# Kernel tuning notes

Measured on AMD Instinct MI355X. Metric: run time of the kernel, lower is better.

## Reference

```python
import math
import jax, jax.numpy as jnp
import numpy as np

BS, H, S, DK = 16, 8, 1024, 128
NEG = -1e32

def setup_inputs() -> dict:
    key = jax.random.key(0)
    kq, kk, kv = jax.random.split(key, 3)
    q = jax.random.normal(kq, (BS, H, S, DK), dtype=jnp.float32)
    k = jax.random.normal(kk, (BS, H, S, DK), dtype=jnp.float32)
    v = jax.random.normal(kv, (BS, H, S, DK), dtype=jnp.float32)
    # causal mask: 1 where attending allowed (lower-triangular incl. diagonal)
    mask = jnp.tril(jnp.ones((S, S), dtype=jnp.int32))[None, None, :, :]
    return {"q": q, "k": k, "v": v, "mask": mask, "k_index": 5}


def reference(q, k, v, mask, k_index):
    d_k = q.shape[-1]
    bs, h, S, _ = q.shape
    # raw scaled scores [bs, h, S, S]
    scores = jnp.einsum("bhqd,bhkd->bhqk", q, k) / math.sqrt(d_k)
    scores = jnp.where(mask == 0, NEG, scores)
    scores = jax.nn.softmax(scores, axis=-1)
    # 'sparseattn' branch: keep rows < k_index intact; for later rows keep only
    # entries >= the k_index-th largest value, then re-softmax everything.
    scores_a = scores[:, :, :k_index, :]
    scores_b = scores[:, :, k_index:, :]
    kth = jax.lax.top_k(scores_b, k_index)[0][..., -1:]  # k-th largest per row
    scores_b = jnp.where(scores_b - kth >= 0, scores_b, NEG)
    scores = jnp.concatenate([scores_a, scores_b], axis=2)
    scores = jax.nn.softmax(scores, axis=-1)
    # zero_pad: zero out attention of the first position
    pad_zero = jnp.zeros((bs, h, 1, S), dtype=scores.dtype)
    scores = jnp.concatenate([pad_zero, scores[:, :, 1:, :]], axis=2)
    # dropout prob is 0.0 -> identity
    out = jnp.einsum("bhqk,bhkd->bhqd", scores, v)
    return out
```

## Files before the change

### kernel.cpp

```cpp
#include <hip/hip_runtime.h>
#include <math.h>

#define BSZ 16
#define NH  8
#define SEQ 1024
#define DK  128
#define QB  64
#define KB  64
#define NT  256
#define TOPK 5
#define NC   8
#define EPS_REF 4e-3f

typedef _Float16 half8 __attribute__((ext_vector_type(8)));
typedef float f32x4 __attribute__((ext_vector_type(4)));

#define INV2P11 4.8828125e-4f

__device__ __forceinline__ void ins8p(float (&t)[NC], int (&ti)[NC], float x, int xi) {
    #pragma unroll
    for (int i = 0; i < NC; ++i) {
        bool gt = x > t[i];
        float tv = t[i]; int tiv = ti[i];
        t[i]  = gt ? x  : tv;
        ti[i] = gt ? xi : tiv;
        x  = gt ? tv  : x;
        xi = gt ? tiv : xi;
    }
}

__device__ __forceinline__ float ref_score(const float* __restrict__ qp,
                                           const float* __restrict__ kp,
                                           float scale) {
    const float4* q4 = (const float4*)qp;
    const float4* k4 = (const float4*)kp;
    float a0 = 0.f;
    #pragma unroll 8
    for (int c = 0; c < DK / 4; ++c) {
        float4 kx = k4[c];
        float4 t0 = q4[c];
        a0 = fmaf(kx.x, t0.x, a0);
        a0 = fmaf(kx.y, t0.y, a0);
        a0 = fmaf(kx.z, t0.z, a0);
        a0 = fmaf(kx.w, t0.w, a0);
    }
    return a0 * scale;
}

__launch_bounds__(NT, 4)
__global__ void attn_topk_mfma(const float* __restrict__ Q,
                               const float* __restrict__ Km,
                               const float* __restrict__ V,
                               const int* __restrict__ kidx_ptr,
                               float* __restrict__ out)
{
    const int bh   = blockIdx.y;
    const int qb   = ((int)gridDim.x - 1 - (int)blockIdx.x) * QB;
    const int tid  = threadIdx.x;
    const int lane = tid & 63;
    const int w    = tid >> 6;
    const int c    = lane & 15;
    const int grp  = lane >> 4;
    const int Kv   = *kidx_ptr;

    __shared__ __align__(16) _Float16 khi [KB * DK];
    __shared__ __align__(16) _Float16 kmid[KB * DK];
    __shared__ float s_coef[4][16][NC];
    __shared__ int   s_idx [4][16][NC];
    __shared__ float s_ext [4][16];
    __shared__ int   s_cnt [4][16];
    __shared__ float s_sv  [DK];
    __shared__ float s_svp [2][DK];

    if (qb == 0) {
        const float* vb = V + (size_t)bh * SEQ * DK;
        const int col = tid & 127, hf = tid >> 7;
        float a = 0.f;
        #pragma unroll 8
        for (int j = hf * 512; j < hf * 512 + 512; ++j)
            a += vb[(size_t)j * DK + col];
        s_svp[hf][col] = a;
        __syncthreads();
        if (tid < DK) s_sv[tid] = s_svp[0][tid] + s_svp[1][tid];
    }

    const int qrow = qb + w * 16 + c;
    const float scale = 0.08838834764831845f;
    half8 qhi[4], qmid[4];
    {
        const float* qp = Q + ((size_t)bh * SEQ + qrow) * DK;
        #pragma unroll
        for (int d = 0; d < 4; ++d) {
            const float4* p4 = (const float4*)(qp + d * 32 + grp * 8);
            float4 f0 = p4[0], f1 = p4[1];
            float v[8] = {f0.x, f0.y, f0.z, f0.w, f1.x, f1.y, f1.z, f1.w};
            #pragma unroll
            for (int j = 0; j < 8; ++j) {
                _Float16 h = (_Float16)v[j];
                float r = v[j] - (float)h;
                qhi[d][j]  = h;
                qmid[d][j] = (_Float16)(r * 2048.0f);
            }
        }
    }

    float t[NC]; int ti[NC];
    #pragma unroll
    for (int i = 0; i < NC; ++i) { t[i] = -INFINITY; ti[i] = 0; }
    float Zr = 0.f;

    const int qmax_w = qb + w * 16 + 15;
    const int ntile  = qb / KB + 1;
    const float* kb_g = Km + (size_t)bh * SEQ * DK;

    for (int kt = 0; kt < ntile; ++kt) {
        __syncthreads();
        {
            const float* src = kb_g + (size_t)kt * KB * DK;
            #pragma unroll
            for (int it = 0; it < 4; ++it) {
                int e   = it * 2048 + tid * 8;
                int row = e >> 7;
                int d0  = e & 127;
                const float4* g4 = (const float4*)(src + (size_t)row * DK + d0);
                float4 f0 = g4[0], f1 = g4[1];
                float v[8] = {f0.x, f0.y, f0.z, f0.w, f1.x, f1.y, f1.z, f1.w};
                half8 hv, mv;
                #pragma unroll
                for (int j = 0; j < 8; ++j) {
                    _Float16 h = (_Float16)v[j];
                    float r = v[j] - (float)h;
                    hv[j] = h;
                    mv[j] = (_Float16)(r * 2048.0f);
                }
                int off = row * 256 + ((d0 * 2) ^ ((row & 7) << 4));
                *(half8*)((char*)khi  + off) = hv;
                *(half8*)((char*)kmid + off) = mv;
            }
        }
        __syncthreads();

        const int kbase_t = kt * KB;
        #pragma unroll
        for (int fr = 0; fr < 4; ++fr) {
            if (kbase_t + fr * 16 <= qmax_w) {
                f32x4 a1 = {0.f, 0.f, 0.f, 0.f};
                f32x4 a2 = {0.f, 0.f, 0.f, 0.f};
                const int kr    = fr * 16 + c;
                const int rbase = kr * 256;
                const int sw    = (kr & 7) << 4;
                #pragma unroll
                for (int d = 0; d < 4; ++d) {
                    int off = rbase + (((d * 64) + grp * 16) ^ sw);
                    half8 ah = *(const half8*)((const char*)khi  + off);
                    half8 am = *(const half8*)((const char*)kmid + off);
                    a1 = __builtin_amdgcn_mfma_f32_16x16x32_f16(ah, qhi[d],  a1, 0, 0, 0);
                    a2 = __builtin_amdgcn_mfma_f32_16x16x32_f16(ah, qmid[d], a2, 0, 0, 0);
                    a2 = __builtin_amdgcn_mfma_f32_16x16x32_f16(am, qhi[d],  a2, 0, 0, 0);
                }
                #pragma unroll
                for (int r = 0; r < 4; ++r) {
                    float s = fmaf(a2[r], INV2P11, a1[r]) * scale;
                    int kg = kbase_t + fr * 16 + grp * 4 + r;
                    if (kg <= qrow) {
                        if (s > t[NC - 1]) {
                            float mo = t[0];
                            ins8p(t, ti, s, kg);
                            float mn = t[0];
                            if (mn != mo) Zr *= __expf(mo - mn);
                        }
                        Zr += __expf(s - t[0]);
                    }
                }
            }
        }
    }

    #pragma unroll
    for (int off = 16; off < 64; off <<= 1) {
        float zo = __shfl_xor(Zr, off, 64);
        float to[NC]; int io[NC];
        #pragma unroll
        for (int i = 0; i < NC; ++i) {
            to[i] = __shfl_xor(t[i], off, 64);
            io[i] = __shfl_xor(ti[i], off, 64);
        }
        float ms = t[0], mo = to[0];
        float mN = fmaxf(ms, mo);
        float fs = (ms == mN) ? 1.f : __expf(ms - mN);
        float fo = (mo == mN) ? 1.f : __expf(mo - mN);
        Zr = Zr * fs + zo * fo;
        #pragma unroll
        for (int i = 0; i < NC; ++i) ins8p(t, ti, to[i], io[i]);
    }

    if (qrow >= Kv && (t[TOPK - 1] - t[TOPK]) < EPS_REF) {
        const float* qrp = Q + ((size_t)bh * SEQ + qrow) * DK;
        float rv0 = -INFINITY, rv1 = -INFINITY;
        int   ri0 = ti[grp * 2], ri1 = ti[grp * 2 + 1];
        if (t[grp * 2] != -INFINITY)
            rv0 = ref_score(qrp, Km + ((size_t)bh * SEQ + ri0) * DK, scale);
        if (t[grp * 2 + 1] != -INFINITY)
            rv1 = ref_score(qrp, Km + ((size_t)bh * SEQ + ri1) * DK, scale);
        float av[NC]; int ai[NC];
        #pragma unroll
        for (int j = 0; j < NC; ++j) {
            int src = (lane & 15) | ((j >> 1) << 4);
            av[j] = __shfl((j & 1) ? rv1 : rv0, src, 64);
            ai[j] = __shfl((j & 1) ? ri1 : ri0, src, 64);
        }
        #pragma unroll
        for (int a = 1; a < NC; ++a) {
            #pragma unroll
            for (int b = NC - 1; b > 0; --b) {
                if (av[b] > av[b - 1]) {
                    float tv = av[b]; av[b] = av[b - 1]; av[b - 1] = tv;
                    int   tj = ai[b]; ai[b] = ai[b - 1]; ai[b - 1] = tj;
                }
            }
        }
        #pragma unroll
        for (int i = 0; i < NC; ++i) { t[i] = av[i]; ti[i] = ai[i]; }
    }

    if (grp == 0) {
        const float m1 = t[0];
        const float invZ = 1.f / Zr;
        if (qrow >= Kv) {
            float p[NC];
            #pragma unroll
            for (int i = 0; i < NC; ++i)
                p[i] = (t[i] == -INFINITY) ? -1.f : expf(t[i] - m1) * invZ;
            const float kth_p = p[TOPK - 1];
            int n = 0; float wsum = 0.f;
            #pragma unroll
            for (int i = 0; i < NC; ++i) {
                if (t[i] != -INFINITY && p[i] >= kth_p) {
                    float wv = expf(p[i]);
                    s_coef[w][c][n] = wv;
                    s_idx [w][c][n] = ti[i];
                    wsum += wv;
                    ++n;
                }
            }
            float iw = 1.f / wsum;
            for (int i = 0; i < n; ++i) s_coef[w][c][i] *= iw;
            s_cnt[w][c] = n;
            s_ext[w][c] = 0.f;
        } else if (qrow == 0) {
            s_cnt[w][c] = 0;
            s_ext[w][c] = 0.f;
        } else {
            float z2 = (float)(SEQ - 1 - qrow);
            float ex[TOPK];
            #pragma unroll
            for (int i = 0; i < TOPK; ++i) {
                if (i <= qrow) {
                    float p = expf(t[i] - m1) * invZ;
                    ex[i] = expf(p);
                    z2 += ex[i];
                } else ex[i] = 0.f;
            }
            float iz = 1.f / z2;
            #pragma unroll
            for (int i = 0; i < TOPK; ++i) {
                if (i <= qrow) {
                    s_coef[w][c][i] = (ex[i] - 1.f) * iz;
                    s_idx [w][c][i] = ti[i];
                }
            }
            s_cnt[w][c] = qrow + 1;
            s_ext[w][c] = iz;
        }
    }
    __syncthreads();

    const float* vb = V + (size_t)bh * SEQ * DK;
    #pragma unroll 2
    for (int r = 0; r < 16; ++r) {
        const int row = qb + w * 16 + r;
        const int n = s_cnt[w][r];
        const float e = s_ext[w][r];
        float a0, a1v;
        if (e != 0.f) { a0 = e * s_sv[2 * lane]; a1v = e * s_sv[2 * lane + 1]; }
        else          { a0 = 0.f; a1v = 0.f; }
        for (int i = 0; i < n; ++i) {
            float cf = s_coef[w][r][i];
            int   ji = s_idx [w][r][i];
            const float2 v2 = *(const float2*)(vb + (size_t)ji * DK + 2 * lane);
            a0  = fmaf(cf, v2.x, a0);
            a1v = fmaf(cf, v2.y, a1v);
        }
        float2 o; o.x = a0; o.y = a1v;
        *(float2*)(out + ((size_t)bh * SEQ + row) * DK + 2 * lane) = o;
    }
}

extern "C" void kernel_launch(void* const* d_in, const int* in_sizes, int n_in,
                              void* d_out, int out_size, void* d_ws, size_t ws_size,
                              hipStream_t stream) {
    const float* q    = (const float*)d_in[0];
    const float* k    = (const float*)d_in[1];
    const float* v    = (const float*)d_in[2];
    const int*   kidx = (const int*)d_in[4];
    float* out = (float*)d_out;

    dim3 grid(SEQ / QB, BSZ * NH);
    attn_topk_mfma<<<grid, NT, 0, stream>>>(q, k, v, kidx, out);
}
```

Before: 511.7 us.

## Prefetch next K tile into registers, specialize diagonal tile, use exp2 softmax

```diff
diff --git a/kernel.cpp b/kernel.cpp
--- a/kernel.cpp
+++ b/kernel.cpp
@@ -10,7 +10,8 @@
 #define NT  256
 #define TOPK 5
 #define NC   8
-#define EPS_REF 4e-3f
+#define EPS_REF 6e-3f
+#define LOG2E 1.4426950408889634f
 
 typedef _Float16 half8 __attribute__((ext_vector_type(8)));
 typedef float f32x4 __attribute__((ext_vector_type(4)));
@@ -60,7 +61,7 @@
     const int lane = tid & 63;
     const int w    = tid >> 6;
     const int c    = lane & 15;
-    const int grp  = lane >> 4;
+    const int g16  = lane >> 4;
     const int Kv   = *kidx_ptr;
 
     __shared__ __align__(16) _Float16 khi [KB * DK];
@@ -85,13 +86,14 @@
     }
 
     const int qrow = qb + w * 16 + c;
-    const float scale = 0.08838834764831845f;
+    const float scale  = 0.08838834764831845f;
+    const float scale2 = 0.08838834764831845f * LOG2E;
     half8 qhi[4], qmid[4];
     {
         const float* qp = Q + ((size_t)bh * SEQ + qrow) * DK;
         #pragma unroll
         for (int d = 0; d < 4; ++d) {
-            const float4* p4 = (const float4*)(qp + d * 32 + grp * 8);
+            const float4* p4 = (const float4*)(qp + d * 32 + g16 * 8);
             float4 f0 = p4[0], f1 = p4[1];
             float v[8] = {f0.x, f0.y, f0.z, f0.w, f1.x, f1.y, f1.z, f1.w};
             #pragma unroll
@@ -107,23 +109,28 @@
     float t[NC]; int ti[NC];
     #pragma unroll
     for (int i = 0; i < NC; ++i) { t[i] = -INFINITY; ti[i] = 0; }
-    float Zr = 0.f;
-
-    const int qmax_w = qb + w * 16 + 15;
+    float Zp0 = 0.f, Zp1 = 0.f, Zp2 = 0.f, Zp3 = 0.f;
+
     const int ntile  = qb / KB + 1;
     const float* kb_g = Km + (size_t)bh * SEQ * DK;
+
+    float4 pf[8];
+    {
+        const float* sp = kb_g + (size_t)(lane >> 2) * DK + w * 32 + (lane & 3) * 8;
+        #pragma unroll
+        for (int it = 0; it < 4; ++it) {
+            const float4* p4 = (const float4*)(sp + (size_t)it * 16 * DK);
+            pf[2 * it]     = p4[0];
+            pf[2 * it + 1] = p4[1];
+        }
+    }
 
     for (int kt = 0; kt < ntile; ++kt) {
         __syncthreads();
         {
-            const float* src = kb_g + (size_t)kt * KB * DK;
             #pragma unroll
             for (int it = 0; it < 4; ++it) {
-                int e   = it * 2048 + tid * 8;
-                int row = e >> 7;
-                int d0  = e & 127;
-                const float4* g4 = (const float4*)(src + (size_t)row * DK + d0);
-                float4 f0 = g4[0], f1 = g4[1];
+                float4 f0 = pf[2 * it], f1 = pf[2 * it + 1];
                 float v[8] = {f0.x, f0.y, f0.z, f0.w, f1.x, f1.y, f1.z, f1.w};
                 half8 hv, mv;
                 #pragma unroll
@@ -133,48 +140,87 @@
                     hv[j] = h;
                     mv[j] = (_Float16)(r * 2048.0f);
                 }
-                int off = row * 256 + ((d0 * 2) ^ ((row & 7) << 4));
+                const int off = it * 4096 + tid * 16;
                 *(half8*)((char*)khi  + off) = hv;
                 *(half8*)((char*)kmid + off) = mv;
             }
         }
+        if (kt + 1 < ntile) {
+            const float* sp = kb_g + (size_t)((kt + 1) * KB + (lane >> 2)) * DK
+                            + w * 32 + (lane & 3) * 8;
+            #pragma unroll
+            for (int it = 0; it < 4; ++it) {
+                const float4* p4 = (const float4*)(sp + (size_t)it * 16 * DK);
+                pf[2 * it]     = p4[0];
+                pf[2 * it + 1] = p4[1];
+            }
+        }
         __syncthreads();
 
         const int kbase_t = kt * KB;
+        const bool lastT = (kt == ntile - 1);
         #pragma unroll
         for (int fr = 0; fr < 4; ++fr) {
-            if (kbase_t + fr * 16 <= qmax_w) {
+            const bool doFull = !lastT || (fr < w);
+            const bool doDiag = lastT && (fr == w);
+            if (doFull | doDiag) {
                 f32x4 a1 = {0.f, 0.f, 0.f, 0.f};
                 f32x4 a2 = {0.f, 0.f, 0.f, 0.f};
-                const int kr    = fr * 16 + c;
-                const int rbase = kr * 256;
-                const int sw    = (kr & 7) << 4;
+                const int rbase = fr * 4096 + c * 64 + g16 * 16;
                 #pragma unroll
                 for (int d = 0; d < 4; ++d) {
-                    int off = rbase + (((d * 64) + grp * 16) ^ sw);
+                    const int off = rbase + d * 1024;
                     half8 ah = *(const half8*)((const char*)khi  + off);
                     half8 am = *(const half8*)((const char*)kmid + off);
                     a1 = __builtin_amdgcn_mfma_f32_16x16x32_f16(ah, qhi[d],  a1, 0, 0, 0);
                     a2 = __builtin_amdgcn_mfma_f32_16x16x32_f16(ah, qmid[d], a2, 0, 0, 0);
                     a2 = __builtin_amdgcn_mfma_f32_16x16x32_f16(am, qhi[d],  a2, 0, 0, 0);
                 }
-                #pragma unroll
-                for (int r = 0; r < 4; ++r) {
-                    float s = fmaf(a2[r], INV2P11, a1[r]) * scale;
-                    int kg = kbase_t + fr * 16 + grp * 4 + r;
-                    if (kg <= qrow) {
+                if (doFull) {
+                    #pragma unroll
+                    for (int r = 0; r < 4; ++r) {
+                        float s = fmaf(a2[r], INV2P11, a1[r]) * scale2;
+                        int kg = kbase_t + fr * 16 + g16 * 4 + r;
                         if (s > t[NC - 1]) {
                             float mo = t[0];
                             ins8p(t, ti, s, kg);
                             float mn = t[0];
-                            if (mn != mo) Zr *= __expf(mo - mn);
+                            if (mn != mo) {
+                                float f = exp2f(mo - mn);
+                                Zp0 *= f; Zp1 *= f; Zp2 *= f; Zp3 *= f;
+                            }
                         }
-                        Zr += __expf(s - t[0]);
+                        float e = exp2f(s - t[0]);
+                        if (r == 0) Zp0 += e; else if (r == 1) Zp1 += e;
+                        else if (r == 2) Zp2 += e; else Zp3 += e;
                     }
-                }
-            }
-        }
-    }
+                } else {
+                    #pragma unroll
+                    for (int r = 0; r < 4; ++r) {
+                        float s = fmaf(a2[r], INV2P11, a1[r]) * scale2;
+                        int kgl = g16 * 4 + r;
+                        if (kgl <= c) {
+                            int kg = kbase_t + fr * 16 + kgl;
+                            if (s > t[NC - 1]) {
+                                float mo = t[0];
+                                ins8p(t, ti, s, kg);
+                                float mn = t[0];
+                                if (mn != mo) {
+                                    float f = exp2f(mo - mn);
+                                    Zp0 *= f; Zp1 *= f; Zp2 *= f; Zp3 *= f;
+                                }
+                            }
+                            float e = exp2f(s - t[0]);
+                            if (r == 0) Zp0 += e; else if (r == 1) Zp1 += e;
+                            else if (r == 2) Zp2 += e; else Zp3 += e;
+                        }
+                    }
+                }
+            }
+        }
+    }
+
+    float Zr = (Zp0 + Zp1) + (Zp2 + Zp3);
 
     #pragma unroll
     for (int off = 16; off < 64; off <<= 1) {
@@ -187,8 +233,8 @@
         }
         float ms = t[0], mo = to[0];
         float mN = fmaxf(ms, mo);
-        float fs = (ms == mN) ? 1.f : __expf(ms - mN);
-        float fo = (mo == mN) ? 1.f : __expf(mo - mN);
+        float fs = (ms == mN) ? 1.f : exp2f(ms - mN);
+        float fo = (mo == mN) ? 1.f : exp2f(mo - mN);
         Zr = Zr * fs + zo * fo;
         #pragma unroll
         for (int i = 0; i < NC; ++i) ins8p(t, ti, to[i], io[i]);
@@ -197,10 +243,10 @@
     if (qrow >= Kv && (t[TOPK - 1] - t[TOPK]) < EPS_REF) {
         const float* qrp = Q + ((size_t)bh * SEQ + qrow) * DK;
         float rv0 = -INFINITY, rv1 = -INFINITY;
-        int   ri0 = ti[grp * 2], ri1 = ti[grp * 2 + 1];
-        if (t[grp * 2] != -INFINITY)
+        int   ri0 = ti[g16 * 2], ri1 = ti[g16 * 2 + 1];
+        if (t[g16 * 2] != -INFINITY)
             rv0 = ref_score(qrp, Km + ((size_t)bh * SEQ + ri0) * DK, scale);
-        if (t[grp * 2 + 1] != -INFINITY)
+        if (t[g16 * 2 + 1] != -INFINITY)
             rv1 = ref_score(qrp, Km + ((size_t)bh * SEQ + ri1) * DK, scale);
         float av[NC]; int ai[NC];
         #pragma unroll
@@ -220,17 +266,17 @@
             }
         }
         #pragma unroll
-        for (int i = 0; i < NC; ++i) { t[i] = av[i]; ti[i] = ai[i]; }
-    }
-
-    if (grp == 0) {
+        for (int i = 0; i < NC; ++i) { t[i] = av[i] * LOG2E; ti[i] = ai[i]; }
+    }
+
+    if (g16 == 0) {
         const float m1 = t[0];
         const float invZ = 1.f / Zr;
         if (qrow >= Kv) {
             float p[NC];
             #pragma unroll
             for (int i = 0; i < NC; ++i)
-                p[i] = (t[i] == -INFINITY) ? -1.f : expf(t[i] - m1) * invZ;
+                p[i] = (t[i] == -INFINITY) ? -1.f : exp2f(t[i] - m1) * invZ;
             const float kth_p = p[TOPK - 1];
             int n = 0; float wsum = 0.f;
             #pragma unroll
@@ -256,7 +302,7 @@
             #pragma unroll
             for (int i = 0; i < TOPK; ++i) {
                 if (i <= qrow) {
-                    float p = expf(t[i] - m1) * invZ;
+                    float p = exp2f(t[i] - m1) * invZ;
                     ex[i] = expf(p);
                     z2 += ex[i];
                 } else ex[i] = 0.f;
```

After: 540.2 us. 5.6% more time.

## Drop online max rescaling, fold scale and log2e into Q, shrink K tile to 32

Applied to the files above, without the earlier changes.

```diff
diff --git a/kernel.cpp b/kernel.cpp
--- a/kernel.cpp
+++ b/kernel.cpp
@@ -6,18 +6,19 @@
 #define SEQ 1024
 #define DK  128
 #define QB  64
-#define KB  64
+#define KB  32
 #define NT  256
 #define TOPK 5
-#define NC   8
-#define EPS_REF 4e-3f
+#define NC   6
+#define EPS_REF 6e-3f
+#define LOG2E 1.4426950408889634f
 
 typedef _Float16 half8 __attribute__((ext_vector_type(8)));
 typedef float f32x4 __attribute__((ext_vector_type(4)));
 
 #define INV2P11 4.8828125e-4f
 
-__device__ __forceinline__ void ins8p(float (&t)[NC], int (&ti)[NC], float x, int xi) {
+__device__ __forceinline__ void ins6p(float (&t)[NC], int (&ti)[NC], float x, int xi) {
     #pragma unroll
     for (int i = 0; i < NC; ++i) {
         bool gt = x > t[i];
@@ -47,7 +48,7 @@
     return a0 * scale;
 }
 
-__launch_bounds__(NT, 4)
+__launch_bounds__(NT, 6)
 __global__ void attn_topk_mfma(const float* __restrict__ Q,
                                const float* __restrict__ Km,
                                const float* __restrict__ V,
@@ -60,7 +61,7 @@
     const int lane = tid & 63;
     const int w    = tid >> 6;
     const int c    = lane & 15;
-    const int grp  = lane >> 4;
+    const int g16  = lane >> 4;
     const int Kv   = *kidx_ptr;
 
     __shared__ __align__(16) _Float16 khi [KB * DK];
@@ -85,19 +86,21 @@
     }
 
     const int qrow = qb + w * 16 + c;
-    const float scale = 0.08838834764831845f;
+    const float scale  = 0.08838834764831845f;
+    const float scale2 = 0.08838834764831845f * LOG2E;
     half8 qhi[4], qmid[4];
     {
         const float* qp = Q + ((size_t)bh * SEQ + qrow) * DK;
         #pragma unroll
         for (int d = 0; d < 4; ++d) {
-            const float4* p4 = (const float4*)(qp + d * 32 + grp * 8);
+            const float4* p4 = (const float4*)(qp + d * 32 + g16 * 8);
             float4 f0 = p4[0], f1 = p4[1];
             float v[8] = {f0.x, f0.y, f0.z, f0.w, f1.x, f1.y, f1.z, f1.w};
             #pragma unroll
             for (int j = 0; j < 8; ++j) {
-                _Float16 h = (_Float16)v[j];
-                float r = v[j] - (float)h;
+                float x = v[j] * scale2;
+                _Float16 h = (_Float16)x;
+                float r = x - (float)h;
                 qhi[d][j]  = h;
                 qmid[d][j] = (_Float16)(r * 2048.0f);
             }
@@ -107,10 +110,10 @@
     float t[NC]; int ti[NC];
     #pragma unroll
     for (int i = 0; i < NC; ++i) { t[i] = -INFINITY; ti[i] = 0; }
-    float Zr = 0.f;
-
-    const int qmax_w = qb + w * 16 + 15;
-    const int ntile  = qb / KB + 1;
+    float Zp0 = 0.f, Zp1 = 0.f, Zp2 = 0.f, Zp3 = 0.f;
+
+    const int R      = (qb >> 4) + w;
+    const int ntile  = qb / KB + 2;
     const float* kb_g = Km + (size_t)bh * SEQ * DK;
 
     for (int kt = 0; kt < ntile; ++kt) {
@@ -118,12 +121,10 @@
         {
             const float* src = kb_g + (size_t)kt * KB * DK;
             #pragma unroll
-            for (int it = 0; it < 4; ++it) {
-                int e   = it * 2048 + tid * 8;
-                int row = e >> 7;
-                int d0  = e & 127;
-                const float4* g4 = (const float4*)(src + (size_t)row * DK + d0);
-                float4 f0 = g4[0], f1 = g4[1];
+            for (int o = 0; o < 2; ++o) {
+                const float* sp = src + (size_t)(o * 16 + c) * DK + w * 32 + g16 * 8;
+                const float4* p4 = (const float4*)sp;
+                float4 f0 = p4[0], f1 = p4[1];
                 float v[8] = {f0.x, f0.y, f0.z, f0.w, f1.x, f1.y, f1.z, f1.w};
                 half8 hv, mv;
                 #pragma unroll
@@ -133,81 +134,75 @@
                     hv[j] = h;
                     mv[j] = (_Float16)(r * 2048.0f);
                 }
-                int off = row * 256 + ((d0 * 2) ^ ((row & 7) << 4));
+                const int off = o * 4096 + w * 1024 + lane * 16;
                 *(half8*)((char*)khi  + off) = hv;
                 *(half8*)((char*)kmid + off) = mv;
             }
         }
         __syncthreads();
 
-        const int kbase_t = kt * KB;
-        #pragma unroll
-        for (int fr = 0; fr < 4; ++fr) {
-            if (kbase_t + fr * 16 <= qmax_w) {
-                f32x4 a1 = {0.f, 0.f, 0.f, 0.f};
-                f32x4 a2 = {0.f, 0.f, 0.f, 0.f};
-                const int kr    = fr * 16 + c;
-                const int rbase = kr * 256;
-                const int sw    = (kr & 7) << 4;
-                #pragma unroll
-                for (int d = 0; d < 4; ++d) {
-                    int off = rbase + (((d * 64) + grp * 16) ^ sw);
-                    half8 ah = *(const half8*)((const char*)khi  + off);
-                    half8 am = *(const half8*)((const char*)kmid + off);
-                    a1 = __builtin_amdgcn_mfma_f32_16x16x32_f16(ah, qhi[d],  a1, 0, 0, 0);
-                    a2 = __builtin_amdgcn_mfma_f32_16x16x32_f16(ah, qmid[d], a2, 0, 0, 0);
-                    a2 = __builtin_amdgcn_mfma_f32_16x16x32_f16(am, qhi[d],  a2, 0, 0, 0);
-                }
-                #pragma unroll
-                for (int r = 0; r < 4; ++r) {
-                    float s = fmaf(a2[r], INV2P11, a1[r]) * scale;
-                    int kg = kbase_t + fr * 16 + grp * 4 + r;
-                    if (kg <= qrow) {
-                        if (s > t[NC - 1]) {
-                            float mo = t[0];
-                            ins8p(t, ti, s, kg);
-                            float mn = t[0];
-                            if (mn != mo) Zr *= __expf(mo - mn);
-                        }
-                        Zr += __expf(s - t[0]);
-                    }
-                }
-            }
-        }
-    }
+        #pragma unroll
+        for (int fr = 0; fr < 2; ++fr) {
+            const int F = kt * 2 + fr;
+            if (F > R) break;
+            const bool diag = (F == R);
+            f32x4 a1 = {0.f, 0.f, 0.f, 0.f};
+            f32x4 a2 = {0.f, 0.f, 0.f, 0.f};
+            const int rbase = fr * 4096 + lane * 16;
+            #pragma unroll
+            for (int d = 0; d < 4; ++d) {
+                const int off = rbase + d * 1024;
+                half8 ah = *(const half8*)((const char*)khi  + off);
+                half8 am = *(const half8*)((const char*)kmid + off);
+                a1 = __builtin_amdgcn_mfma_f32_16x16x32_f16(ah, qhi[d],  a1, 0, 0, 0);
+                a2 = __builtin_amdgcn_mfma_f32_16x16x32_f16(ah, qmid[d], a2, 0, 0, 0);
+                a2 = __builtin_amdgcn_mfma_f32_16x16x32_f16(am, qhi[d],  a2, 0, 0, 0);
+            }
+            #pragma unroll
+            for (int r = 0; r < 4; ++r) {
+                float s = fmaf(a2[r], INV2P11, a1[r]);
+                int kgl = g16 * 4 + r;
+                if (!diag || kgl <= c) {
+                    int kg = F * 16 + kgl;
+                    if (s > t[NC - 1]) ins6p(t, ti, s, kg);
+                    float e = exp2f(s);
+                    if (r == 0) Zp0 += e; else if (r == 1) Zp1 += e;
+                    else if (r == 2) Zp2 += e; else Zp3 += e;
+                }
+            }
+        }
+    }
+
+    float Zr = (Zp0 + Zp1) + (Zp2 + Zp3);
 
     #pragma unroll
     for (int off = 16; off < 64; off <<= 1) {
-        float zo = __shfl_xor(Zr, off, 64);
+        Zr += __shfl_xor(Zr, off, 64);
         float to[NC]; int io[NC];
         #pragma unroll
         for (int i = 0; i < NC; ++i) {
             to[i] = __shfl_xor(t[i], off, 64);
             io[i] = __shfl_xor(ti[i], off, 64);
         }
-        float ms = t[0], mo = to[0];
-        float mN = fmaxf(ms, mo);
-        float fs = (ms == mN) ? 1.f : __expf(ms - mN);
-        float fo = (mo == mN) ? 1.f : __expf(mo - mN);
-        Zr = Zr * fs + zo * fo;
-        #pragma unroll
-        for (int i = 0; i < NC; ++i) ins8p(t, ti, to[i], io[i]);
+        #pragma unroll
+        for (int i = 0; i < NC; ++i) ins6p(t, ti, to[i], io[i]);
     }
 
     if (qrow >= Kv && (t[TOPK - 1] - t[TOPK]) < EPS_REF) {
         const float* qrp = Q + ((size_t)bh * SEQ + qrow) * DK;
         float rv0 = -INFINITY, rv1 = -INFINITY;
-        int   ri0 = ti[grp * 2], ri1 = ti[grp * 2 + 1];
-        if (t[grp * 2] != -INFINITY)
+        int   ri0 = ti[g16];
+        int   ri1 = (g16 < 2) ? ti[4 + g16] : 0;
+        if (t[g16] != -INFINITY)
             rv0 = ref_score(qrp, Km + ((size_t)bh * SEQ + ri0) * DK, scale);
-        if (t[grp * 2 + 1] != -INFINITY)
+        if (g16 < 2 && t[4 + g16] != -INFINITY)
             rv1 = ref_score(qrp, Km + ((size_t)bh * SEQ + ri1) * DK, scale);
         float av[NC]; int ai[NC];
         #pragma unroll
         for (int j = 0; j < NC; ++j) {
-            int src = (lane & 15) | ((j >> 1) << 4);
-            av[j] = __shfl((j & 1) ? rv1 : rv0, src, 64);
-            ai[j] = __shfl((j & 1) ? ri1 : ri0, src, 64);
+            int src = (lane & 15) | ((j < 4 ? j : j - 4) << 4);
+            av[j] = __shfl(j < 4 ? rv0 : rv1, src, 64);
+            ai[j] = __shfl(j < 4 ? ri0 : ri1, src, 64);
         }
         #pragma unroll
         for (int a = 1; a < NC; ++a) {
@@ -220,17 +215,16 @@
             }
         }
         #pragma unroll
-        for (int i = 0; i < NC; ++i) { t[i] = av[i]; ti[i] = ai[i]; }
-    }
-
-    if (grp == 0) {
-        const float m1 = t[0];
+        for (int i = 0; i < NC; ++i) { t[i] = av[i] * LOG2E; ti[i] = ai[i]; }
+    }
+
+    if (g16 == 0) {
         const float invZ = 1.f / Zr;
         if (qrow >= Kv) {
             float p[NC];
             #pragma unroll
             for (int i = 0; i < NC; ++i)
-                p[i] = (t[i] == -INFINITY) ? -1.f : expf(t[i] - m1) * invZ;
+                p[i] = (t[i] == -INFINITY) ? -1.f : exp2f(t[i]) * invZ;
             const float kth_p = p[TOPK - 1];
             int n = 0; float wsum = 0.f;
             #pragma unroll
@@ -256,7 +250,7 @@
             #pragma unroll
             for (int i = 0; i < TOPK; ++i) {
                 if (i <= qrow) {
-                    float p = expf(t[i] - m1) * invZ;
+                    float p = exp2f(t[i]) * invZ;
                     ex[i] = expf(p);
                     z2 += ex[i];
                 } else ex[i] = 0.f;
```

After: 513.3 us. Within noise of the previous version (+0.3%).
